# Performance work log

Hardware: AMD Instinct MI355X
Metric: run time of the kernel (lower is better)

Reference implementation:

```python
import jax, jax.numpy as jnp
import numpy as np

N_NODES = 100000
N_EDGES = 1600000
N_FEATS = 9
HIDDEN = 64
DIM_OUT = 1
N_GRAPHS = 512
EPS_MSG = 1e-7   # GENConv message eps
BN_EPS = 1e-5    # BatchNorm1d eps


def _lin(key, fan_in, fan_out):
    kw, kb = jax.random.split(key)
    s = 1.0 / np.sqrt(fan_in)
    w = jax.random.uniform(kw, (fan_in, fan_out), jnp.float32, -s, s)
    b = jax.random.uniform(kb, (fan_out,), jnp.float32, -s, s)
    return w, b


def setup_inputs() -> dict:
    key = jax.random.key(0)
    ks = jax.random.split(key, 32)
    inp = {}
    inp["x"] = jax.random.normal(ks[0], (N_NODES, N_FEATS), jnp.float32)
    inp["edge_index"] = jax.random.randint(ks[1], (2, N_EDGES), 0, N_NODES, jnp.int64)
    inp["batch_idx"] = jnp.sort(jax.random.randint(ks[2], (N_NODES,), 0, N_GRAPHS, jnp.int64))
    # conv1 input projections (in != out)
    inp["w_src"], inp["b_src"] = _lin(ks[3], N_FEATS, HIDDEN)
    inp["w_dst"], inp["b_dst"] = _lin(ks[4], N_FEATS, HIDDEN)
    # per-conv MLP: Linear(H,2H) -> BN(2H) -> ReLU -> Linear(2H,H)
    for i, k in zip((1, 2, 3), (ks[5], ks[6], ks[7])):
        k1, k2 = jax.random.split(k)
        w1, b1 = _lin(k1, HIDDEN, 2 * HIDDEN)
        w2, b2 = _lin(k2, 2 * HIDDEN, HIDDEN)
        inp[f"w1_{i}"], inp[f"b1_{i}"] = w1, b1
        inp[f"g_{i}"] = jnp.ones((2 * HIDDEN,), jnp.float32)
        inp[f"be_{i}"] = jnp.zeros((2 * HIDDEN,), jnp.float32)
        inp[f"w2_{i}"], inp[f"b2_{i}"] = w2, b2
    inp["w_dense"], inp["b_dense"] = _lin(ks[8], HIDDEN, DIM_OUT)
    return inp


def _seg_softmax(m, idx, n):
    # per-channel softmax over edges sharing the same destination node
    mx = jax.ops.segment_max(m, idx, num_segments=n)
    e = jnp.exp(m - mx[idx])
    s = jax.ops.segment_sum(e, idx, num_segments=n)
    return e / (s[idx] + 1e-16)


def _mlp(h, w1, b1, g, be, w2, b2):
    h = h @ w1 + b1                                   # [N, 2H]
    mu = jnp.mean(h, axis=0)
    var = jnp.var(h, axis=0)
    h = (h - mu) * jax.lax.rsqrt(var + BN_EPS) * g + be
    return jax.nn.relu(h) @ w2 + b2                   # [N, H]


def _genconv(x_src, x_dst, src, dst, w1, b1, g, be, w2, b2):
    n = x_dst.shape[0]
    msg = jax.nn.relu(x_src[src]) + EPS_MSG           # [E, H] gather + message
    alpha = _seg_softmax(msg, dst, n)                 # softmax aggregation, t=1
    aggr = jax.ops.segment_sum(alpha * msg, dst, num_segments=n)
    return _mlp(aggr + x_dst, w1, b1, g, be, w2, b2)


def reference(x, edge_index, batch_idx, w_src, b_src, w_dst, b_dst,
              w1_1, b1_1, g_1, be_1, w2_1, b2_1,
              w1_2, b1_2, g_2, be_2, w2_2, b2_2,
              w1_3, b1_3, g_3, be_3, w2_3, b2_3,
              w_dense, b_dense):
    src, dst = edge_index[0], edge_index[1]
    h = jax.nn.relu(_genconv(x @ w_src + b_src, x @ w_dst + b_dst, src, dst,
                             w1_1, b1_1, g_1, be_1, w2_1, b2_1))
    h = jax.nn.relu(_genconv(h, h, src, dst, w1_2, b1_2, g_2, be_2, w2_2, b2_2))
    h = jax.nn.relu(_genconv(h, h, src, dst, w1_3, b1_3, g_3, be_3, w2_3, b2_3))
    # global mean pool over graphs
    tot = jax.ops.segment_sum(h, batch_idx, num_segments=N_GRAPHS)
    cnt = jax.ops.segment_sum(jnp.ones((h.shape[0],), h.dtype), batch_idx, num_segments=N_GRAPHS)
    pooled = tot / jnp.maximum(cnt, 1.0)[:, None]     # [G, H]
    return jax.nn.sigmoid(pooled @ w_dense + b_dense) # [G, 1]
```

## Files before the change

kernel.cpp:

```cpp
#include <hip/hip_runtime.h>

typedef unsigned short ushort_t;
typedef __attribute__((ext_vector_type(8))) short bf16x8;
typedef __attribute__((ext_vector_type(4))) float f32x4;
typedef __attribute__((ext_vector_type(4))) int int4v;

__device__ __forceinline__ unsigned short f2bf(float f){
  unsigned u = __float_as_uint(f);
  u = (u + 0x7FFFu + ((u >> 16) & 1u)) >> 16;
  return (unsigned short)u;
}
__device__ __forceinline__ float bf2f(unsigned short h){
  return __uint_as_float(((unsigned)h) << 16);
}


__global__ __launch_bounds__(256) void k_bhist(const int* __restrict__ dst, int* __restrict__ bcnt,
                                               int E, int NB){
  __shared__ int l[512];
  int t = threadIdx.x;
  for(int b=t; b<NB; b+=256) l[b] = 0;
  __syncthreads();
  int base = blockIdx.x*4096 + t*16;
  if(base + 16 <= E){
    #pragma unroll
    for(int r=0;r<4;++r){
      int4v d = __builtin_nontemporal_load((const int4v*)(dst + base + r*4));
      atomicAdd(&l[d.x >> 8], 1); atomicAdd(&l[d.y >> 8], 1);
      atomicAdd(&l[d.z >> 8], 1); atomicAdd(&l[d.w >> 8], 1);
    }
  } else {
    for(int i=base; i<E; ++i) atomicAdd(&l[dst[i] >> 8], 1);
  }
  __syncthreads();
  for(int b=t; b<NB; b+=256){
    int c = l[b];
    if(c) atomicAdd(&bcnt[b], c);
  }
}

__global__ __launch_bounds__(512) void k_bscan(const int* __restrict__ bcnt, int* __restrict__ bbase,
                                               int* __restrict__ bcur, int* __restrict__ rp,
                                               int NB, int N, int E){
  __shared__ int s[512];
  int t = threadIdx.x;
  int v = (t < NB) ? bcnt[t] : 0;
  s[t] = v;
  __syncthreads();
  for(int off=1; off<512; off<<=1){
    int x = 0;
    if(t >= off) x = s[t-off];
    __syncthreads();
    if(t >= off) s[t] += x;
    __syncthreads();
  }
  int excl = s[t] - v;
  if(t < NB){ bbase[t] = excl; bcur[t] = excl; }
  if(t == NB-1) bbase[NB] = excl + v;
  if(t == 0) rp[N] = E;
}

__global__ __launch_bounds__(256) void k_part(const int* __restrict__ src, const int* __restrict__ dst,
                                              int* __restrict__ bcur, unsigned* __restrict__ ebuf,
                                              int E, int NB){
  __shared__ int lcnt[512];
  __shared__ int lbase[512];
  int t = threadIdx.x;
  int base = blockIdx.x*4096 + t*16;
  for(int b=t; b<NB; b+=256) lcnt[b] = 0;
  __syncthreads();

  int srcv[16], dstv[16];
  if(base + 16 <= E){
    #pragma unroll
    for(int r=0;r<4;++r){
      *(int4v*)(dstv + r*4) = __builtin_nontemporal_load((const int4v*)(dst + base + r*4));
      *(int4v*)(srcv + r*4) = __builtin_nontemporal_load((const int4v*)(src + base + r*4));
    }
  } else {
    #pragma unroll
    for(int k=0;k<16;++k){
      int i = base + k;
      if(i < E){ dstv[k] = dst[i]; srcv[k] = src[i]; }
      else dstv[k] = -1;
    }
  }
  #pragma unroll
  for(int r=0;r<16;++r)
    if(dstv[r] >= 0) atomicAdd(&lcnt[dstv[r] >> 8], 1);
  __syncthreads();
  for(int b=t; b<NB; b+=256){
    int c = lcnt[b];
    lbase[b] = c ? atomicAdd(&bcur[b], c) : 0;
    lcnt[b] = 0;
  }
  __syncthreads();
  #pragma unroll
  for(int r=0;r<16;++r){
    if(dstv[r] >= 0){
      int b = dstv[r] >> 8;
      int p = lbase[b] + atomicAdd(&lcnt[b], 1);
      ebuf[p] = (((unsigned)dstv[r] & 255u) << 17) | (unsigned)srcv[r];
    }
  }
}

__global__ __launch_bounds__(256) void k_place(const int* __restrict__ bbase, const unsigned* __restrict__ ebuf,
                                               int* __restrict__ esrc, int* __restrict__ rp, int N){
  __shared__ int lcnt[256];
  __shared__ int sc[256];
  __shared__ int lcur[256];
  int t = threadIdx.x;
  int b = blockIdx.x;
  int n0 = b << 8;
  int e0 = bbase[b], e1 = bbase[b+1];
  lcnt[t] = 0;
  __syncthreads();
  for(int i = e0 + t; i < e1; i += 256)
    atomicAdd(&lcnt[ebuf[i] >> 17], 1);
  __syncthreads();
  int v = lcnt[t];
  sc[t] = v;
  __syncthreads();
  for(int off=1; off<256; off<<=1){
    int x = 0;
    if(t >= off) x = sc[t-off];
    __syncthreads();
    if(t >= off) sc[t] += x;
    __syncthreads();
  }
  int rpv = e0 + sc[t] - v;
  if(n0 + t < N) rp[n0 + t] = rpv;
  lcur[t] = rpv;
  __syncthreads();
  for(int i = e0 + t; i < e1; i += 256){
    unsigned w = ebuf[i];
    int dl = (int)(w >> 17);
    int p = atomicAdd(&lcur[dl], 1);
    esrc[p] = (int)(w & 0x1FFFFu);
  }
}

__global__ __launch_bounds__(256) void k_wconv(const float* __restrict__ w1a, const float* __restrict__ w2a,
                                               const float* __restrict__ w1b, const float* __restrict__ w2b,
                                               const float* __restrict__ w1c, const float* __restrict__ w2c,
                                               ushort_t* __restrict__ w1t, ushort_t* __restrict__ w2t){
  int L = blockIdx.x >> 6;
  const float* w1 = (L==0) ? w1a : (L==1) ? w1b : w1c;
  const float* w2 = (L==0) ? w2a : (L==1) ? w2b : w2c;
  int t = (blockIdx.x & 63)*256 + threadIdx.x;
  if(t < 8192){
    int n = t >> 6, k = t & 63;
    w1t[L*8192 + n*64 + k] = f2bf(w1[k*128 + n]);
  } else {
    int i = t - 8192;
    int n = i >> 7, k = i & 127;
    w2t[L*8192 + n*128 + k] = f2bf(w2[k*64 + n]);
  }
}

__global__ __launch_bounds__(256) void k_proj(const float* __restrict__ x,
                                              const float* __restrict__ ws, const float* __restrict__ bs,
                                              const float* __restrict__ wd, const float* __restrict__ bd,
                                              ushort_t* __restrict__ hd16, ushort_t* __restrict__ gs16, int N){
  int gid = blockIdx.x*256 + threadIdx.x;
  int n = gid >> 6, c = gid & 63;
  if(n >= N) return;
  float as = bs[c], ad = bd[c];
  const float* xr = x + (size_t)n*9;
  #pragma unroll
  for(int k=0;k<9;++k){
    float xv = xr[k];
    as += xv * ws[k*64 + c];
    ad += xv * wd[k*64 + c];
  }
  hd16[(size_t)n*64 + c] = f2bf(ad);
  gs16[(size_t)n*64 + c] = f2bf(fmaxf(as, 0.f));
}

__global__ __launch_bounds__(256) void k_emlp1(const ushort_t* __restrict__ gs, const ushort_t* __restrict__ xd16,
                                               const int* __restrict__ rp, const int* __restrict__ es,
                                               const ushort_t* __restrict__ w1t, const float* __restrict__ b1,
                                               ushort_t* __restrict__ h1, float* __restrict__ bnp, int N){
  __shared__ ushort_t yt[32*72];
  __shared__ ushort_t cs[32*136];
  int t = threadIdx.x;
  int w = t >> 6, lane = t & 63;
  int nbase = blockIdx.x * 32;

  const ushort_t* gl = gs + lane;
  for(int i=0;i<8;++i){
    int nl = w*8 + i;
    int n = nbase + nl;
    float aggr = 0.f;
    if(n < N){
      int beg = __builtin_amdgcn_readfirstlane(rp[n]);
      int end = __builtin_amdgcn_readfirstlane(rp[n+1]);
      float S[8], T[8];
      #pragma unroll
      for(int j=0;j<8;++j){ S[j]=0.f; T[j]=0.f; }
      int nfull = beg + ((end - beg) & ~7);
      int base = beg;
      for(; base < nfull; base += 8){
        float g[8];
        #pragma unroll
        for(int j=0;j<8;++j){
          int idx = __builtin_amdgcn_readfirstlane(es[base+j]);
          g[j] = bf2f(gl[(size_t)idx*64]) + 1e-7f;
        }
        #pragma unroll
        for(int j=0;j<8;++j){
          float p = __expf(g[j]);
          S[j] += p; T[j] += p*g[j];
        }
      }
      if(base < end){
        float g[8];
        #pragma unroll
        for(int j=0;j<8;++j){
          int e = base + j;
          int idx = __builtin_amdgcn_readfirstlane(es[e < end ? e : end-1]);
          g[j] = bf2f(gl[(size_t)idx*64]) + 1e-7f;
        }
        #pragma unroll
        for(int j=0;j<8;++j){
          float p = (base + j < end) ? __expf(g[j]) : 0.f;
          S[j] += p; T[j] += p*g[j];
        }
      }
      float Ss = ((S[0]+S[1])+(S[2]+S[3])) + ((S[4]+S[5])+(S[6]+S[7]));
      float Ts = ((T[0]+T[1])+(T[2]+T[3])) + ((T[4]+T[5])+(T[6]+T[7]));
      aggr = Ts/(Ss + 1e-16f) + bf2f(xd16[(size_t)n*64 + lane]);
    }
    yt[nl*72 + lane] = f2bf(aggr);
  }
  __syncthreads();

  int ln = lane & 15, quad = lane >> 4;
  bf16x8 B[2][2];
  #pragma unroll
  for(int c=0;c<2;++c){
    int n = (2*w+c)*16 + ln;
    #pragma unroll
    for(int q=0;q<2;++q)
      B[c][q] = *(const bf16x8*)(w1t + n*64 + q*32 + quad*8);
  }

  f32x4 z = {0.f,0.f,0.f,0.f};
  f32x4 acc[2][2] = {{z,z},{z,z}};
  #pragma unroll
  for(int q=0;q<2;++q){
    #pragma unroll
    for(int tt=0;tt<2;++tt){
      bf16x8 A = *(const bf16x8*)(yt + (tt*16 + ln)*72 + q*32 + quad*8);
      #pragma unroll
      for(int c=0;c<2;++c)
        acc[tt][c] = __builtin_amdgcn_mfma_f32_16x16x32_bf16(A, B[c][q], acc[tt][c], 0,0,0);
    }
  }

  float s[2] = {0.f, 0.f}, qq[2] = {0.f, 0.f};
  #pragma unroll
  for(int c=0;c<2;++c){
    int n = (2*w+c)*16 + ln;
    float bb = b1[n];
    #pragma unroll
    for(int tt=0;tt<2;++tt){
      #pragma unroll
      for(int r=0;r<4;++r){
        int row = tt*16 + quad*4 + r;
        float v = acc[tt][c][r] + bb;
        bool ok = (nbase + row) < N;
        s[c]  += ok ? v   : 0.f;
        qq[c] += ok ? v*v : 0.f;
        cs[row*136 + n] = f2bf(v);
      }
    }
  }
  {
    float* slice = bnp + (size_t)(blockIdx.x & 31)*256;
    #pragma unroll
    for(int c=0;c<2;++c){
      float vs = s[c], vq = qq[c];
      vs += __shfl_down(vs, 32, 64); vs += __shfl_down(vs, 16, 64);
      vq += __shfl_down(vq, 32, 64); vq += __shfl_down(vq, 16, 64);
      if(quad == 0){
        int col = (2*w+c)*16 + ln;
        atomicAdd(&slice[col], vs);
        atomicAdd(&slice[128+col], vq);
      }
    }
  }
  __syncthreads();
  #pragma unroll
  for(int r2=0;r2<2;++r2){
    int idx = r2*256 + t;
    int row = idx >> 4, c8 = (idx & 15)*8;
    int m = nbase + row;
    if(m < N)
      *(uint4*)(h1 + (size_t)m*128 + c8) = *(const uint4*)(cs + row*136 + c8);
  }
}

__global__ __launch_bounds__(128) void k_bnfold(float* __restrict__ bnp, const float* __restrict__ g,
                                                const float* __restrict__ be, float* __restrict__ sb, float invN){
  int j = threadIdx.x;
  float s = 0.f, q = 0.f;
  for(int b=0;b<32;++b){ s += bnp[b*256 + j]; q += bnp[b*256 + 128 + j]; }
  float mu = s*invN;
  float var = q*invN - mu*mu;
  float sc = g[j] * rsqrtf(var + 1e-5f);
  sb[j] = sc;
  sb[128+j] = be[j] - mu*sc;
  for(int b=0;b<32;++b){ bnp[b*256 + j] = 0.f; bnp[b*256 + 128 + j] = 0.f; }
}

__global__ __launch_bounds__(256) void k_mlp2(const ushort_t* __restrict__ h1, const float* __restrict__ sb,
                                              const ushort_t* __restrict__ w2t, const float* __restrict__ b2,
                                              ushort_t* __restrict__ h16, int N){
  __shared__ ushort_t act[64*136];
  __shared__ ushort_t cs2[64*72];
  int t = threadIdx.x;
  int n0 = blockIdx.x*64;
  #pragma unroll
  for(int r=0;r<4;++r){
    int idx = r*256 + t;
    int row = idx >> 4, k8 = (idx & 15)*8;
    int n = n0 + row;
    ushort_t tmp[8];
    if(n < N){
      *(uint4*)tmp = *(const uint4*)(h1 + (size_t)n*128 + k8);
    } else {
      #pragma unroll
      for(int j=0;j<8;++j) tmp[j] = 0;
    }
    #pragma unroll
    for(int j=0;j<8;++j){
      float v = bf2f(tmp[j]) * sb[k8+j] + sb[128+k8+j];
      tmp[j] = f2bf(fmaxf(v, 0.f));
    }
    *(uint4*)(act + row*136 + k8) = *(uint4*)tmp;
  }
  __syncthreads();
  int w = t >> 6, lane = t & 63;
  int ln = lane & 15, quad = lane >> 4;

  int n = w*16 + ln;
  bf16x8 B[4];
  #pragma unroll
  for(int q=0;q<4;++q)
    B[q] = *(const bf16x8*)(w2t + n*128 + q*32 + quad*8);

  f32x4 z = {0.f,0.f,0.f,0.f};
  f32x4 acc[4] = {z,z,z,z};
  #pragma unroll
  for(int q=0;q<4;++q){
    #pragma unroll
    for(int tt=0;tt<4;++tt){
      bf16x8 A = *(const bf16x8*)(act + (tt*16 + ln)*136 + q*32 + quad*8);
      acc[tt] = __builtin_amdgcn_mfma_f32_16x16x32_bf16(A, B[q], acc[tt], 0,0,0);
    }
  }
  float bb = b2[n];
  #pragma unroll
  for(int tt=0;tt<4;++tt){
    #pragma unroll
    for(int r=0;r<4;++r){
      int row = tt*16 + quad*4 + r;
      float v = fmaxf(acc[tt][r] + bb, 0.f);
      cs2[row*72 + n] = f2bf(v);
    }
  }
  __syncthreads();
  #pragma unroll
  for(int r2=0;r2<2;++r2){
    int idx = r2*256 + t;
    int row = idx >> 3, c8 = (idx & 7)*8;
    int m = n0 + row;
    if(m < N)
      *(uint4*)(h16 + (size_t)m*64 + c8) = *(const uint4*)(cs2 + row*72 + c8);
  }
}

__device__ __forceinline__ int lbound(const int* a, int n, int key){
  int lo = 0, hi = n;
  while(lo < hi){
    int mid = (lo + hi) >> 1;
    if(a[mid] < key) lo = mid + 1; else hi = mid;
  }
  return lo;
}

__global__ __launch_bounds__(256) void k_pool(const ushort_t* __restrict__ h16, const int* __restrict__ batch,
                                              const float* __restrict__ wd, const float* __restrict__ bd,
                                              float* __restrict__ out, int N){
  int g = blockIdx.x;
  int lo = lbound(batch, N, g);
  int hi = lbound(batch, N, g+1);
  int c = threadIdx.x & 63, w = threadIdx.x >> 6;
  float acc = 0.f;
  for(int n = lo + w; n < hi; n += 4) acc += bf2f(h16[(size_t)n*64 + c]);
  __shared__ float red[4][64];
  red[w][c] = acc;
  __syncthreads();
  if(w == 0){
    float v = red[0][c] + red[1][c] + red[2][c] + red[3][c];
    float count = (float)(hi - lo);
    v = v / fmaxf(count, 1.f) * wd[c];
    for(int off=32; off>0; off>>=1) v += __shfl_down(v, off, 64);
    if(c == 0) out[g] = 1.f / (1.f + expf(-(v + bd[0])));
  }
}


extern "C" void kernel_launch(void* const* d_in, const int* in_sizes, int n_in,
                              void* d_out, int out_size, void* d_ws, size_t ws_size,
                              hipStream_t stream){
  const float* x      = (const float*)d_in[0];
  const int*   ei     = (const int*)  d_in[1];
  const int*   batch  = (const int*)  d_in[2];
  const float* w_src  = (const float*)d_in[3];
  const float* b_src  = (const float*)d_in[4];
  const float* w_dst  = (const float*)d_in[5];
  const float* b_dst  = (const float*)d_in[6];
  const float* w_dense= (const float*)d_in[25];
  const float* b_dense= (const float*)d_in[26];
  float* out = (float*)d_out;

  const int N = in_sizes[2];
  const int E = in_sizes[1] / 2;
  const int* src = ei;
  const int* dst = ei + E;

  char* ws = (char*)d_ws;
  size_t off = 0;
  auto take = [&](size_t bytes) -> void* {
    void* p = ws + off;
    off += (bytes + 255) & ~(size_t)255;
    return p;
  };
  ushort_t* hd16 = (ushort_t*)take((size_t)N*64*2);
  ushort_t* gs16 = (ushort_t*)take((size_t)N*64*2);
  ushort_t* h1   = (ushort_t*)take((size_t)N*128*2);
  ushort_t* h16  = (ushort_t*)take((size_t)N*64*2);
  unsigned* ebuf = (unsigned*)take((size_t)E*4);
  int*      esrc = (int*)     take((size_t)E*4);
  int*      rp   = (int*)     take((size_t)(N+1)*4);
  int*      bcnt = (int*)     take(512*4);
  float*    bnp  = (float*)   take(32*256*4);
  int*      bbase= (int*)     take(520*4);
  int*      bcur = (int*)     take(512*4);
  float*    sb   = (float*)   take(256*4);
  ushort_t* w1t  = (ushort_t*)take(3*8192*2);
  ushort_t* w2t  = (ushort_t*)take(3*8192*2);

  const int nblk1 = (N + 31) / 32;
  const int gN64  = (N*64 + 255) / 256;
  const int NB    = (N + 255) >> 8;
  const int nchnk = (E + 4095) / 4096;

  k_wconv<<<192, 256, 0, stream>>>(
    (const float*)d_in[7],  (const float*)d_in[11],
    (const float*)d_in[13], (const float*)d_in[17],
    (const float*)d_in[19], (const float*)d_in[23],
    w1t, w2t);

  (void)hipMemsetAsync(bcnt, 0, 512*4 + 32*256*4, stream);

  k_bhist<<<nchnk, 256, 0, stream>>>(dst, bcnt, E, NB);
  k_bscan<<<1,     512, 0, stream>>>(bcnt, bbase, bcur, rp, NB, N, E);
  k_part <<<nchnk, 256, 0, stream>>>(src, dst, bcur, ebuf, E, NB);
  k_place<<<NB,    256, 0, stream>>>(bbase, ebuf, esrc, rp, N);

  k_proj<<<gN64, 256, 0, stream>>>(x, w_src, b_src, w_dst, b_dst, hd16, gs16, N);

  const ushort_t* gs_l[3] = { gs16, h16, h16 };
  const ushort_t* xd_l[3] = { hd16, h16, h16 };
  const float invN = 1.0f / (float)N;

  for(int L=0; L<3; ++L){
    const float* b1 = (const float*)d_in[7 + 6*L + 1];
    const float* g  = (const float*)d_in[7 + 6*L + 2];
    const float* be = (const float*)d_in[7 + 6*L + 3];
    const float* b2 = (const float*)d_in[7 + 6*L + 5];

    k_emlp1<<<nblk1, 256, 0, stream>>>(gs_l[L], xd_l[L], rp, esrc, w1t + L*8192, b1, h1, bnp, N);
    k_bnfold<<<1, 128, 0, stream>>>(bnp, g, be, sb, invN);
    k_mlp2<<<(N+63)/64, 256, 0, stream>>>(h1, sb, w2t + L*8192, b2, h16, N);
  }

  k_pool<<<512, 256, 0, stream>>>(h16, batch, w_dense, b_dense, out, N);
}
```

Before: 429.4 us.

## Fuse small kernels to cut launch count: scan into histogram, BN fold into MLP2

The histogram kernel now runs the bucket scan itself, using a last-block ticket, so the separate scan launch goes away. The weight conversion and input projection kernels become one launch, and the BatchNorm fold is recomputed per block inside k_mlp2, with per-layer stat buffers zeroed by a single upfront memset. The message epsilon is also pulled out of the per-edge loop algebraically. Together these remove about five small launches and their serialisation gaps, at the cost of each mlp2 block redundantly reading 32x256 partial stats.

```diff
diff --git a/kernel.cpp b/kernel.cpp
--- a/kernel.cpp
+++ b/kernel.cpp
@@ -16,10 +16,16 @@
 
 
 __global__ __launch_bounds__(256) void k_bhist(const int* __restrict__ dst, int* __restrict__ bcnt,
-                                               int E, int NB){
+                                               int* __restrict__ ticket,
+                                               int* __restrict__ bbase, int* __restrict__ bcur,
+                                               int* __restrict__ rp,
+                                               int E, int NB, int N, int nblk){
   __shared__ int l[512];
+  __shared__ int sA[512];
+  __shared__ int sB[512];
+  __shared__ int isLast;
   int t = threadIdx.x;
-  for(int b=t; b<NB; b+=256) l[b] = 0;
+  for(int b=t; b<512; b+=256) l[b] = 0;
   __syncthreads();
   int base = blockIdx.x*4096 + t*16;
   if(base + 16 <= E){
@@ -37,26 +43,36 @@
     int c = l[b];
     if(c) atomicAdd(&bcnt[b], c);
   }
-}
-
-__global__ __launch_bounds__(512) void k_bscan(const int* __restrict__ bcnt, int* __restrict__ bbase,
-                                               int* __restrict__ bcur, int* __restrict__ rp,
-                                               int NB, int N, int E){
-  __shared__ int s[512];
-  int t = threadIdx.x;
-  int v = (t < NB) ? bcnt[t] : 0;
-  s[t] = v;
-  __syncthreads();
+  __threadfence();
+  if(t == 0) isLast = (atomicAdd(ticket, 1) == nblk - 1);
+  __syncthreads();
+  if(!isLast) return;
+
+  int orig[2];
+  for(int r=0;r<2;++r){
+    int i = r*256 + t;
+    orig[r] = (i < NB) ? atomicAdd(&bcnt[i], 0) : 0;
+    sA[i] = orig[r];
+  }
+  __syncthreads();
+  int* cur = sA; int* nxt = sB;
   for(int off=1; off<512; off<<=1){
-    int x = 0;
-    if(t >= off) x = s[t-off];
+    for(int r=0;r<2;++r){
+      int i = r*256 + t;
+      nxt[i] = (i >= off) ? cur[i] + cur[i-off] : cur[i];
+    }
     __syncthreads();
-    if(t >= off) s[t] += x;
-    __syncthreads();
-  }
-  int excl = s[t] - v;
-  if(t < NB){ bbase[t] = excl; bcur[t] = excl; }
-  if(t == NB-1) bbase[NB] = excl + v;
+    int* tmp = cur; cur = nxt; nxt = tmp;
+  }
+  for(int r=0;r<2;++r){
+    int i = r*256 + t;
+    if(i < NB){
+      int excl = cur[i] - orig[r];
+      bbase[i] = excl;
+      bcur[i]  = excl;
+      if(i == NB-1) bbase[NB] = excl + orig[r];
+    }
+  }
   if(t == 0) rp[N] = E;
 }
 
@@ -141,29 +157,30 @@
   }
 }
 
-__global__ __launch_bounds__(256) void k_wconv(const float* __restrict__ w1a, const float* __restrict__ w2a,
-                                               const float* __restrict__ w1b, const float* __restrict__ w2b,
-                                               const float* __restrict__ w1c, const float* __restrict__ w2c,
-                                               ushort_t* __restrict__ w1t, ushort_t* __restrict__ w2t){
-  int L = blockIdx.x >> 6;
-  const float* w1 = (L==0) ? w1a : (L==1) ? w1b : w1c;
-  const float* w2 = (L==0) ? w2a : (L==1) ? w2b : w2c;
-  int t = (blockIdx.x & 63)*256 + threadIdx.x;
-  if(t < 8192){
-    int n = t >> 6, k = t & 63;
-    w1t[L*8192 + n*64 + k] = f2bf(w1[k*128 + n]);
-  } else {
-    int i = t - 8192;
-    int n = i >> 7, k = i & 127;
-    w2t[L*8192 + n*128 + k] = f2bf(w2[k*64 + n]);
-  }
-}
-
-__global__ __launch_bounds__(256) void k_proj(const float* __restrict__ x,
+__global__ __launch_bounds__(256) void k_init(const float* __restrict__ w1a, const float* __restrict__ w2a,
+                                              const float* __restrict__ w1b, const float* __restrict__ w2b,
+                                              const float* __restrict__ w1c, const float* __restrict__ w2c,
+                                              ushort_t* __restrict__ w1t, ushort_t* __restrict__ w2t,
+                                              const float* __restrict__ x,
                                               const float* __restrict__ ws, const float* __restrict__ bs,
                                               const float* __restrict__ wd, const float* __restrict__ bd,
                                               ushort_t* __restrict__ hd16, ushort_t* __restrict__ gs16, int N){
-  int gid = blockIdx.x*256 + threadIdx.x;
+  if(blockIdx.x < 192){
+    int L = blockIdx.x >> 6;
+    const float* w1 = (L==0) ? w1a : (L==1) ? w1b : w1c;
+    const float* w2 = (L==0) ? w2a : (L==1) ? w2b : w2c;
+    int t = (blockIdx.x & 63)*256 + threadIdx.x;
+    if(t < 8192){
+      int n = t >> 6, k = t & 63;
+      w1t[L*8192 + n*64 + k] = f2bf(w1[k*128 + n]);
+    } else {
+      int i = t - 8192;
+      int n = i >> 7, k = i & 127;
+      w2t[L*8192 + n*128 + k] = f2bf(w2[k*64 + n]);
+    }
+    return;
+  }
+  int gid = (blockIdx.x - 192)*256 + threadIdx.x;
   int n = gid >> 6, c = gid & 63;
   if(n >= N) return;
   float as = bs[c], ad = bd[c];
@@ -206,7 +223,7 @@
         #pragma unroll
         for(int j=0;j<8;++j){
           int idx = __builtin_amdgcn_readfirstlane(es[base+j]);
-          g[j] = bf2f(gl[(size_t)idx*64]) + 1e-7f;
+          g[j] = bf2f(gl[(size_t)idx*64]);
         }
         #pragma unroll
         for(int j=0;j<8;++j){
@@ -220,7 +237,7 @@
         for(int j=0;j<8;++j){
           int e = base + j;
           int idx = __builtin_amdgcn_readfirstlane(es[e < end ? e : end-1]);
-          g[j] = bf2f(gl[(size_t)idx*64]) + 1e-7f;
+          g[j] = bf2f(gl[(size_t)idx*64]);
         }
         #pragma unroll
         for(int j=0;j<8;++j){
@@ -230,7 +247,7 @@
       }
       float Ss = ((S[0]+S[1])+(S[2]+S[3])) + ((S[4]+S[5])+(S[6]+S[7]));
       float Ts = ((T[0]+T[1])+(T[2]+T[3])) + ((T[4]+T[5])+(T[6]+T[7]));
-      aggr = Ts/(Ss + 1e-16f) + bf2f(xd16[(size_t)n*64 + lane]);
+      aggr = (Ts + 1e-7f*Ss)/(Ss + 1e-16f) + bf2f(xd16[(size_t)n*64 + lane]);
     }
     yt[nl*72 + lane] = f2bf(aggr);
   }
@@ -302,25 +319,25 @@
   }
 }
 
-__global__ __launch_bounds__(128) void k_bnfold(float* __restrict__ bnp, const float* __restrict__ g,
-                                                const float* __restrict__ be, float* __restrict__ sb, float invN){
-  int j = threadIdx.x;
-  float s = 0.f, q = 0.f;
-  for(int b=0;b<32;++b){ s += bnp[b*256 + j]; q += bnp[b*256 + 128 + j]; }
-  float mu = s*invN;
-  float var = q*invN - mu*mu;
-  float sc = g[j] * rsqrtf(var + 1e-5f);
-  sb[j] = sc;
-  sb[128+j] = be[j] - mu*sc;
-  for(int b=0;b<32;++b){ bnp[b*256 + j] = 0.f; bnp[b*256 + 128 + j] = 0.f; }
-}
-
-__global__ __launch_bounds__(256) void k_mlp2(const ushort_t* __restrict__ h1, const float* __restrict__ sb,
+__global__ __launch_bounds__(256) void k_mlp2(const ushort_t* __restrict__ h1, const float* __restrict__ bnp,
+                                              const float* __restrict__ g, const float* __restrict__ be,
                                               const ushort_t* __restrict__ w2t, const float* __restrict__ b2,
-                                              ushort_t* __restrict__ h16, int N){
+                                              ushort_t* __restrict__ h16, float invN, int N){
+  __shared__ float sbl[256];
   __shared__ ushort_t act[64*136];
   __shared__ ushort_t cs2[64*72];
   int t = threadIdx.x;
+  if(t < 128){
+    float s = 0.f, q = 0.f;
+    #pragma unroll 4
+    for(int b=0;b<32;++b){ s += bnp[b*256 + t]; q += bnp[b*256 + 128 + t]; }
+    float mu = s*invN;
+    float var = q*invN - mu*mu;
+    float sc = g[t] * rsqrtf(var + 1e-5f);
+    sbl[t] = sc;
+    sbl[128+t] = be[t] - mu*sc;
+  }
+  __syncthreads();
   int n0 = blockIdx.x*64;
   #pragma unroll
   for(int r=0;r<4;++r){
@@ -336,7 +353,7 @@
     }
     #pragma unroll
     for(int j=0;j<8;++j){
-      float v = bf2f(tmp[j]) * sb[k8+j] + sb[128+k8+j];
+      float v = bf2f(tmp[j]) * sbl[k8+j] + sbl[128+k8+j];
       tmp[j] = f2bf(fmaxf(v, 0.f));
     }
     *(uint4*)(act + row*136 + k8) = *(uint4*)tmp;
@@ -446,11 +463,11 @@
   unsigned* ebuf = (unsigned*)take((size_t)E*4);
   int*      esrc = (int*)     take((size_t)E*4);
   int*      rp   = (int*)     take((size_t)(N+1)*4);
-  int*      bcnt = (int*)     take(512*4);
-  float*    bnp  = (float*)   take(32*256*4);
+  int*      bcnt = (int*)     take(512*4 + 64*4 + 3*32*256*4);
+  int*      ticket = bcnt + 512;
+  float*    bnp  = (float*)(ticket + 64);
   int*      bbase= (int*)     take(520*4);
   int*      bcur = (int*)     take(512*4);
-  float*    sb   = (float*)   take(256*4);
   ushort_t* w1t  = (ushort_t*)take(3*8192*2);
   ushort_t* w2t  = (ushort_t*)take(3*8192*2);
 
@@ -458,21 +475,20 @@
   const int gN64  = (N*64 + 255) / 256;
   const int NB    = (N + 255) >> 8;
   const int nchnk = (E + 4095) / 4096;
-
-  k_wconv<<<192, 256, 0, stream>>>(
+  const size_t zbytes = 512*4 + 64*4 + 3*32*256*4;
+
+  (void)hipMemsetAsync(bcnt, 0, zbytes, stream);
+
+  k_bhist<<<nchnk, 256, 0, stream>>>(dst, bcnt, ticket, bbase, bcur, rp, E, NB, N, nchnk);
+  k_part <<<nchnk, 256, 0, stream>>>(src, dst, bcur, ebuf, E, NB);
+  k_place<<<NB,    256, 0, stream>>>(bbase, ebuf, esrc, rp, N);
+
+  k_init<<<192 + gN64, 256, 0, stream>>>(
     (const float*)d_in[7],  (const float*)d_in[11],
     (const float*)d_in[13], (const float*)d_in[17],
     (const float*)d_in[19], (const float*)d_in[23],
-    w1t, w2t);
-
-  (void)hipMemsetAsync(bcnt, 0, 512*4 + 32*256*4, stream);
-
-  k_bhist<<<nchnk, 256, 0, stream>>>(dst, bcnt, E, NB);
-  k_bscan<<<1,     512, 0, stream>>>(bcnt, bbase, bcur, rp, NB, N, E);
-  k_part <<<nchnk, 256, 0, stream>>>(src, dst, bcur, ebuf, E, NB);
-  k_place<<<NB,    256, 0, stream>>>(bbase, ebuf, esrc, rp, N);
-
-  k_proj<<<gN64, 256, 0, stream>>>(x, w_src, b_src, w_dst, b_dst, hd16, gs16, N);
+    w1t, w2t,
+    x, w_src, b_src, w_dst, b_dst, hd16, gs16, N);
 
   const ushort_t* gs_l[3] = { gs16, h16, h16 };
   const ushort_t* xd_l[3] = { hd16, h16, h16 };
@@ -483,10 +499,10 @@
     const float* g  = (const float*)d_in[7 + 6*L + 2];
     const float* be = (const float*)d_in[7 + 6*L + 3];
     const float* b2 = (const float*)d_in[7 + 6*L + 5];
-
-    k_emlp1<<<nblk1, 256, 0, stream>>>(gs_l[L], xd_l[L], rp, esrc, w1t + L*8192, b1, h1, bnp, N);
-    k_bnfold<<<1, 128, 0, stream>>>(bnp, g, be, sb, invN);
-    k_mlp2<<<(N+63)/64, 256, 0, stream>>>(h1, sb, w2t + L*8192, b2, h16, N);
+    float* bnpL = bnp + (size_t)L*32*256;
+
+    k_emlp1<<<nblk1, 256, 0, stream>>>(gs_l[L], xd_l[L], rp, esrc, w1t + L*8192, b1, h1, bnpL, N);
+    k_mlp2<<<(N+63)/64, 256, 0, stream>>>(h1, bnpL, g, be, w2t + L*8192, b2, h16, invN, N);
   }
 
   k_pool<<<512, 256, 0, stream>>>(h16, batch, w_dense, b_dense, out, N);
```

New measurement: 452.2 us. 5.3% more time.
